# Performance work log

Measured on AMD Instinct MI355X. Metric: run time of the kernel, lower is better.

Reference implementation:

```python
import jax, jax.numpy as jnp
import numpy as np

B, C, T = 32, 32, 1024
K = 64          # kernel_size
DIL = 1         # dilation
MLP_DIM = 256
HID = 256       # mlp_hidden_dim; TanhBlock dims: 256 -> 256 -> 128 -> 1
NF = min(MLP_DIM, K // 2 + 1)          # 33 rfft bins kept
FFT_DIM = C * NF * 2                   # 2112
N_WIN = T - DIL * (K - 1)              # 961 windows


def setup_inputs() -> dict:
    key = jax.random.key(0)
    ks = jax.random.split(key, 8)
    s = 0.02
    return {
        "x": jax.random.normal(ks[0], (B, C, T), dtype=jnp.float32),
        "Wp": jax.random.normal(ks[1], (MLP_DIM, FFT_DIM), dtype=jnp.float32) * s,
        "bp": jnp.zeros((MLP_DIM,), dtype=jnp.float32),
        "W1": jax.random.normal(ks[2], (HID, MLP_DIM), dtype=jnp.float32) * s,
        "b1": jnp.zeros((HID,), dtype=jnp.float32),
        "W2": jax.random.normal(ks[3], (HID // 2, HID), dtype=jnp.float32) * s,
        "b2": jnp.zeros((HID // 2,), dtype=jnp.float32),
        "Wout": jax.random.normal(ks[4], (1, HID // 2), dtype=jnp.float32) * s,
        "bout": jnp.zeros((1,), dtype=jnp.float32),
        "agg": jnp.zeros((N_WIN,), dtype=jnp.float32),
    }


def reference(x, Wp, bp, W1, b1, W2, b2, Wout, bout, agg):
    # Gather all dilated windows at once: window t uses indices (t-start)+k*DIL.
    base = jnp.arange(N_WIN)[:, None] + jnp.arange(K)[None, :] * DIL  # [W, K]
    win = x[:, :, base]                          # [B, C, W, K]
    fft = jnp.fft.rfft(win, axis=-1)[..., :NF]   # [B, C, W, NF] complex
    mag = jnp.log1p(jnp.abs(fft))
    ph = jnp.angle(fft) / np.pi
    feat = jnp.stack([mag, ph], axis=-1)         # [B, C, W, NF, 2]
    # torch reshape order is (C, NF, 2) -> move window axis before channel
    feat = feat.transpose(0, 2, 1, 3, 4).reshape(B, N_WIN, FFT_DIM)  # [B, W, FFT_DIM]
    proj = jnp.tanh(feat @ Wp.T + bp) * np.pi    # [B, W, MLP_DIM]
    h = jnp.tanh(proj @ W1.T + b1)               # [B, W, HID]
    h = jnp.tanh(h @ W2.T + b2)                  # [B, W, HID//2]
    out = (h @ Wout.T + bout)[..., 0]            # [B, W]
    wts = jax.nn.softmax(agg)                    # [W]
    return (out * wts[None, :]).sum(axis=1)      # [B]
```

## Files before the change

kernel.cpp:

```cpp
#include <hip/hip_runtime.h>
#include <math.h>

#define B_   32
#define C_   32
#define T_   1024
#define NF_  33
#define F2_  66
#define FD_  2112
#define NW_  961
#define MLP_ 256
#define HID_ 256
#define HH_  128
#define TN_  32
#define NT_  31

#define PI_F     3.14159265358979323846f
#define LN2_F    0.69314718055994530942f
#define L2E2_F   2.88539008177792681472f

typedef unsigned short u16;
typedef unsigned int   u32;
typedef __attribute__((ext_vector_type(8))) short bf16x8;
typedef __attribute__((ext_vector_type(4))) float f32x4;

__device__ __forceinline__ u16 f2bf(float f) {
    u32 u = __float_as_uint(f);
    u = u + 0x7FFFu + ((u >> 16) & 1u);
    return (u16)(u >> 16);
}
__device__ __forceinline__ float bf2f(u16 h) {
    return __uint_as_float((u32)h << 16);
}
__device__ __forceinline__ void gload16(const void* g, void* l) {
    __builtin_amdgcn_global_load_lds(
        (const __attribute__((address_space(1))) void*)g,
        (__attribute__((address_space(3))) void*)l, 16, 0, 0);
}
__device__ __forceinline__ float ftanh(float x) {
    float z = __builtin_amdgcn_exp2f(x * L2E2_F);
    return 1.f - 2.f * __builtin_amdgcn_rcpf(z + 1.f);
}
__device__ __forceinline__ float flog1p(float x) {
    return __builtin_amdgcn_logf(1.f + x) * LN2_F;
}
__device__ __forceinline__ float fatan2pi(float y, float x) {
    const float ay = fabsf(y), ax = fabsf(x);
    const float mn = fminf(ay, ax), mx = fmaxf(ay, ax);
    float t = mn * __builtin_amdgcn_rcpf(mx);
    t = (mx == 0.f) ? 0.f : t;
    const float s = t * t;
    float p = -0.00373098f;
    p = fmaf(p, s,  0.01676008f);
    p = fmaf(p, s, -0.03706162f);
    p = fmaf(p, s,  0.06160679f);
    p = fmaf(p, s, -0.10587735f);
    p = fmaf(p, s,  0.31830265f);
    p *= t;
    p = (ay > ax) ? 0.5f - p : p;
    p = (x < 0.f) ? 1.0f - p : p;
    return copysignf(p, y);
}

__global__ __launch_bounds__(256) void prep_kernel(
        const float* __restrict__ Wp, const float* __restrict__ W1,
        const float* __restrict__ W2, const float* __restrict__ agg,
        u16* __restrict__ WpH, u16* __restrict__ W1H, u16* __restrict__ W2H,
        float* __restrict__ wts) {
    const int blk = blockIdx.x;
    const int tid = threadIdx.x;
    if (blk < 128) {
        const int total = MLP_ * FD_;
        for (int i = blk * 256 + tid; i < total; i += 128 * 256)
            WpH[i] = f2bf(Wp[i]);
    } else if (blk < 160) {
        const int total = HID_ * MLP_;
        for (int i = (blk - 128) * 256 + tid; i < total; i += 32 * 256)
            W1H[i] = f2bf(W1[i]);
    } else if (blk < 176) {
        const int total = HH_ * HID_;
        for (int i = (blk - 160) * 256 + tid; i < total; i += 16 * 256)
            W2H[i] = f2bf(W2[i]);
    } else {
        __shared__ float red[256];
        float mx = -INFINITY;
        for (int i = tid; i < NW_; i += 256) mx = fmaxf(mx, agg[i]);
        red[tid] = mx; __syncthreads();
        for (int s = 128; s > 0; s >>= 1) {
            if (tid < s) red[tid] = fmaxf(red[tid], red[tid + s]);
            __syncthreads();
        }
        mx = red[0]; __syncthreads();
        float sm = 0.f;
        for (int i = tid; i < NW_; i += 256) sm += expf(agg[i] - mx);
        red[tid] = sm; __syncthreads();
        for (int s = 128; s > 0; s >>= 1) {
            if (tid < s) red[tid] += red[tid + s];
            __syncthreads();
        }
        const float inv = 1.f / red[0];
        for (int i = tid; i < NW_; i += 256) wts[i] = expf(agg[i] - mx) * inv;
    }
}

__global__ __launch_bounds__(256) void feat_kernel(const float* __restrict__ x,
                                                   u32* __restrict__ featP) {
    const int n0 = blockIdx.x * TN_;
    const int cg = blockIdx.y;
    const int bb = blockIdx.z;
    const int tid = threadIdx.x;
    const int tf = tid & 31;
    const int c8 = tid >> 5;
    const int c  = cg * 8 + c8;

    __shared__ float2 stab[64];
    __shared__ float xs[8][96];
    __shared__ float basisT[64][68];

    if (tid < 64) {
        float s, cc;
        sincosf(-PI_F * (float)tid / 32.0f, &s, &cc);
        stab[tid] = make_float2(cc, s);
    }
    __syncthreads();
    for (int e = tid; e < 2048; e += 256) {
        const int f = e >> 6, k = e & 63;
        const float2 w = stab[(f * k) & 63];
        basisT[k][2 * f]     = w.x;
        basisT[k][2 * f + 1] = w.y;
    }
    if (tid < 192) {
        const int cs = tid / 24, q = tid % 24;
        const int t0 = n0 + q * 4;
        const float* xb = x + ((size_t)bb * C_ + cg * 8 + cs) * T_;
        float4 v;
        if (t0 + 3 < T_) {
            v = *(const float4*)(xb + t0);
        } else {
            v.x = (t0 + 0 < T_) ? xb[t0 + 0] : 0.f;
            v.y = (t0 + 1 < T_) ? xb[t0 + 1] : 0.f;
            v.z = (t0 + 2 < T_) ? xb[t0 + 2] : 0.f;
            v.w = 0.f;
        }
        *(float4*)&xs[cs][q * 4] = v;
    }
    __syncthreads();

    const size_t rowb = (size_t)bb * NW_;

    {
        float re = 0.f, im = 0.f;
#pragma unroll
        for (int k = 0; k < 64; ++k) {
            const float xv = xs[c8][k];
            const float2 w = *(const float2*)&basisT[k][2 * tf];
            re = fmaf(xv, w.x, re);
            im = fmaf(xv, w.y, im);
        }
        const float2 st = stab[tf];
        const float cx = st.x, sx = -st.y;

        for (int j = 0; j < TN_; ++j) {
            const int gn = n0 + j;
            if (gn >= NW_) break;
            const float r   = __builtin_amdgcn_sqrtf(re * re + im * im);
            const float mag = flog1p(r);
            const float ph  = fatan2pi(im, re);
            featP[(rowb + gn) * (FD_ / 2) + 33 * c + tf] =
                (u32)f2bf(mag) | ((u32)f2bf(ph) << 16);
            const float tre = re - xs[c8][j] + xs[c8][j + 64];
            re = tre * cx - im * sx;
            im = tre * sx + im * cx;
        }
    }

    {
        const int j   = tid & 31;
        const int c8n = tid >> 5;
        const int gn  = n0 + j;
        if (gn < NW_) {
            float s = 0.f;
#pragma unroll
            for (int k = 0; k < 32; ++k)
                s += xs[c8n][j + 2 * k] - xs[c8n][j + 2 * k + 1];
            const float a = flog1p(fabsf(s));
            const float p = (__float_as_uint(s) >> 31) ? 1.0f : 0.0f;
            featP[(rowb + gn) * (FD_ / 2) + 33 * (cg * 8 + c8n) + 32] =
                (u32)f2bf(a) | ((u32)f2bf(p) << 16);
        }
    }
}

__global__ __launch_bounds__(512, 2) void gemm1t_kernel(
        const u16* __restrict__ A, const u16* __restrict__ BH,
        const float* __restrict__ bias, float scale,
        u16* __restrict__ outH, int Mvalid, int Kd) {
    constexpr int STEPB = 8192 + 16384;
    __shared__ char lds[3 * STEPB];

    const int bm = blockIdx.x;
    const int tid = threadIdx.x;
    const int lane = tid & 63, w = tid >> 6;
    const int wr = w >> 2, wc = w & 3;
    const int m0 = bm * 128;

    f32x4 acc[4][4];
#pragma unroll
    for (int i = 0; i < 4; ++i)
#pragma unroll
        for (int j = 0; j < 4; ++j) acc[i][j] = (f32x4){0.f, 0.f, 0.f, 0.f};

    const size_t rs = (size_t)Kd * 2;
    const char* gA = (const char*)A + (size_t)m0 * rs;
    const char* gB = (const char*)BH;

    auto st1 = [&](const char* g, char* l, int idx) {
        const int row = idx >> 2;
        const int kc  = (idx & 3) ^ ((row >> 1) & 3);
        gload16(g + (size_t)row * rs + (size_t)(kc << 4), l + idx * 16);
    };
    auto stage = [&](int buf, int t) {
        const size_t k0b = (size_t)t << 6;
        char* lb = lds + buf * STEPB;
        st1(gA + k0b, lb, tid);
        st1(gB + k0b, lb + 8192, tid);
        st1(gB + k0b, lb + 8192, tid + 512);
    };

    const int ra_ = wr * 64 + (lane & 15);
    const int rb_ = wc * 64 + (lane & 15);
    const int q   = lane >> 4;
    const int abase = ra_ * 64 + ((q ^ ((ra_ >> 1) & 3)) << 4);
    const int bbase = rb_ * 64 + ((q ^ ((rb_ >> 1) & 3)) << 4);

    const int nt = Kd >> 5;

    stage(0, 0);
    stage(1, 1);

    int cur = 0;
    for (int t = 0; t < nt; ++t) {
        if (t + 1 < nt)
            asm volatile("s_waitcnt vmcnt(3)" ::: "memory");
        else
            asm volatile("s_waitcnt vmcnt(0)" ::: "memory");
        __builtin_amdgcn_sched_barrier(0);
        __builtin_amdgcn_s_barrier();
        asm volatile("" ::: "memory");

        int pf = cur + 2; if (pf >= 3) pf -= 3;
        if (t + 2 < nt) stage(pf, t + 2);

        const char* lb = lds + cur * STEPB;
        bf16x8 a4[4], b4[4];
#pragma unroll
        for (int f = 0; f < 4; ++f) {
            a4[f] = *(const bf16x8*)(lb + abase + f * 1024);
            b4[f] = *(const bf16x8*)(lb + 8192 + bbase + f * 1024);
        }
        __builtin_amdgcn_s_setprio(1);
#pragma unroll
        for (int fm = 0; fm < 4; ++fm)
#pragma unroll
            for (int fn = 0; fn < 4; ++fn)
                acc[fm][fn] = __builtin_amdgcn_mfma_f32_16x16x32_bf16(a4[fm], b4[fn], acc[fm][fn], 0, 0, 0);
        __builtin_amdgcn_s_setprio(0);
        ++cur; if (cur >= 3) cur -= 3;
    }

    float bv[4];
#pragma unroll
    for (int fn = 0; fn < 4; ++fn) bv[fn] = bias[wc * 64 + fn * 16 + (lane & 15)];
#pragma unroll
    for (int fm = 0; fm < 4; ++fm) {
        const int rbase = m0 + wr * 64 + fm * 16 + (lane >> 4) * 4;
#pragma unroll
        for (int fn = 0; fn < 4; ++fn) {
            const int col = wc * 64 + fn * 16 + (lane & 15);
#pragma unroll
            for (int r = 0; r < 4; ++r) {
                const int row = rbase + r;
                if (row < Mvalid) {
                    const float v = ftanh(acc[fm][fn][r] + bv[fn]) * scale;
                    outH[(size_t)row * 256 + col] = f2bf(v);
                }
            }
        }
    }
}

__global__ __launch_bounds__(256, 2) void gemm3f_kernel(
        const u16* __restrict__ A, const u16* __restrict__ BH,
        const float* __restrict__ b2, const float* __restrict__ Wout,
        const float* __restrict__ bout, const float* __restrict__ wts,
        float* __restrict__ partial, int Mvalid, int Kd) {
    constexpr int STEPB = 8192 + 8192;
    __shared__ char lds[3 * STEPB];

    const int bm = blockIdx.x;
    const int tid = threadIdx.x;
    const int lane = tid & 63, w = tid >> 6;
    const int wr = w >> 1, wc = w & 1;
    const int m0 = bm * 128;

    f32x4 acc[4][4];
#pragma unroll
    for (int i = 0; i < 4; ++i)
#pragma unroll
        for (int j = 0; j < 4; ++j) acc[i][j] = (f32x4){0.f, 0.f, 0.f, 0.f};

    const size_t rs = (size_t)Kd * 2;
    const char* gA = (const char*)A + (size_t)m0 * rs;
    const char* gB = (const char*)BH;

    auto st1 = [&](const char* g, char* l, int idx) {
        const int row = idx >> 2;
        const int kc  = (idx & 3) ^ ((row >> 1) & 3);
        gload16(g + (size_t)row * rs + (size_t)(kc << 4), l + idx * 16);
    };
    auto stage = [&](int buf, int t) {
        const size_t k0b = (size_t)t << 6;
        char* lb = lds + buf * STEPB;
        st1(gA + k0b, lb, tid);
        st1(gA + k0b, lb, tid + 256);
        st1(gB + k0b, lb + 8192, tid);
        st1(gB + k0b, lb + 8192, tid + 256);
    };

    const int ra_ = wr * 64 + (lane & 15);
    const int rb_ = wc * 64 + (lane & 15);
    const int q   = lane >> 4;
    const int abase = ra_ * 64 + ((q ^ ((ra_ >> 1) & 3)) << 4);
    const int bbase = rb_ * 64 + ((q ^ ((rb_ >> 1) & 3)) << 4);

    const int nt = Kd >> 5;

    stage(0, 0);
    stage(1, 1);

    int cur = 0;
    for (int t = 0; t < nt; ++t) {
        if (t + 1 < nt)
            asm volatile("s_waitcnt vmcnt(4)" ::: "memory");
        else
            asm volatile("s_waitcnt vmcnt(0)" ::: "memory");
        __builtin_amdgcn_sched_barrier(0);
        __builtin_amdgcn_s_barrier();
        asm volatile("" ::: "memory");

        int pf = cur + 2; if (pf >= 3) pf -= 3;
        if (t + 2 < nt) stage(pf, t + 2);

        const char* lb = lds + cur * STEPB;
        bf16x8 a4[4], b4[4];
#pragma unroll
        for (int f = 0; f < 4; ++f) {
            a4[f] = *(const bf16x8*)(lb + abase + f * 1024);
            b4[f] = *(const bf16x8*)(lb + 8192 + bbase + f * 1024);
        }
        __builtin_amdgcn_s_setprio(1);
#pragma unroll
        for (int fm = 0; fm < 4; ++fm)
#pragma unroll
            for (int fn = 0; fn < 4; ++fn)
                acc[fm][fn] = __builtin_amdgcn_mfma_f32_16x16x32_bf16(a4[fm], b4[fn], acc[fm][fn], 0, 0, 0);
        __builtin_amdgcn_s_setprio(0);
        ++cur; if (cur >= 3) cur -= 3;
    }

    __syncthreads();
    float* rsum = (float*)lds;
    float* red  = (float*)(lds + 1024);

    float bv[4], wv[4];
#pragma unroll
    for (int fn = 0; fn < 4; ++fn) {
        const int col = wc * 64 + fn * 16 + (lane & 15);
        bv[fn] = b2[col];
        wv[fn] = Wout[col];
    }
#pragma unroll
    for (int fm = 0; fm < 4; ++fm) {
#pragma unroll
        for (int r = 0; r < 4; ++r) {
            float c = 0.f;
#pragma unroll
            for (int fn = 0; fn < 4; ++fn)
                c += ftanh(acc[fm][fn][r] + bv[fn]) * wv[fn];
            c += __shfl_xor(c, 1);
            c += __shfl_xor(c, 2);
            c += __shfl_xor(c, 4);
            c += __shfl_xor(c, 8);
            if ((lane & 15) == 0)
                rsum[(wr * 64 + fm * 16 + (lane >> 4) * 4 + r) * 2 + wc] = c;
        }
    }
    __syncthreads();

    const float bO = bout[0];
    float val = 0.f;
    int rowb = -1;
    if (tid < 128) {
        const int gr = m0 + tid;
        if (gr < Mvalid) {
            const float dot = rsum[tid * 2] + rsum[tid * 2 + 1] + bO;
            rowb = gr / NW_;
            val = dot * wts[gr - rowb * NW_];
        }
    }
    __syncthreads();

    const int bFirst = m0 / NW_;
    red[tid] = (tid < 128 && rowb == bFirst) ? val : 0.f;
    __syncthreads();
    for (int s = 128; s > 0; s >>= 1) {
        if (tid < s) red[tid] += red[tid + s];
        __syncthreads();
    }
    if (tid == 0) partial[bm * 2] = red[0];
    __syncthreads();
    red[tid] = (tid < 128 && rowb == bFirst + 1) ? val : 0.f;
    __syncthreads();
    for (int s = 128; s > 0; s >>= 1) {
        if (tid < s) red[tid] += red[tid + s];
        __syncthreads();
    }
    if (tid == 0) partial[bm * 2 + 1] = red[0];
}

__global__ __launch_bounds__(64) void finred_kernel(const float* __restrict__ partial,
                                                    float* __restrict__ out,
                                                    int nbat, int nblocks) {
    const int b = threadIdx.x;
    if (b >= nbat) return;
    int lo = (b * NW_) / 128;
    int hi = ((b + 1) * NW_ - 1) / 128;
    if (hi > nblocks - 1) hi = nblocks - 1;
    float s = 0.f;
    for (int bm = lo; bm <= hi; ++bm) {
        const int slot = ((bm * 128) / NW_ == b) ? 0 : 1;
        s += partial[bm * 2 + slot];
    }
    out[b] = s;
}

extern "C" void kernel_launch(void* const* d_in, const int* in_sizes, int n_in,
                              void* d_out, int out_size, void* d_ws, size_t ws_size,
                              hipStream_t stream) {
    const float* x    = (const float*)d_in[0];
    const float* Wp   = (const float*)d_in[1];
    const float* bp   = (const float*)d_in[2];
    const float* W1   = (const float*)d_in[3];
    const float* b1   = (const float*)d_in[4];
    const float* W2   = (const float*)d_in[5];
    const float* b2   = (const float*)d_in[6];
    const float* Wout = (const float*)d_in[7];
    const float* bout = (const float*)d_in[8];
    const float* agg  = (const float*)d_in[9];
    float* out = (float*)d_out;

    char* wsb = (char*)d_ws;
    size_t off = 0;
    auto ra = [](size_t b) { return (b + 255) & ~(size_t)255; };
    auto alloc = [&](size_t bytes) -> char* {
        char* p = wsb + off;
        off += ra(bytes);
        return p;
    };

    u16* WpH = (u16*)alloc((size_t)MLP_ * FD_ * 2);
    u16* W1H = (u16*)alloc((size_t)HID_ * MLP_ * 2);
    u16* W2H = (u16*)alloc((size_t)HH_ * HID_ * 2);
    float* wts = (float*)alloc((size_t)NW_ * 4);

    const size_t fixed = off;
    int NB = 32;
    for (;;) {
        const size_t M = (size_t)NB * NW_;
        const size_t Mp = ((M + 127) / 128) * 128;
        const size_t need = ra(Mp * FD_ * 2) +
                            ra(Mp * 256 * 2) +
                            ra(Mp * 256 * 2) +
                            ra((Mp / 128) * 2 * 4);
        if (fixed + need <= ws_size || NB == 1) break;
        NB >>= 1;
    }
    const size_t Mmax  = (size_t)NB * NW_;
    const size_t MpMax = ((Mmax + 127) / 128) * 128;
    u16* featH = (u16*)alloc(MpMax * FD_ * 2);
    u16* projH = (u16*)alloc(MpMax * 256 * 2);
    u16* h1H   = (u16*)alloc(MpMax * 256 * 2);
    float* partial = (float*)alloc((MpMax / 128) * 2 * 4);

    prep_kernel<<<dim3(177), dim3(256), 0, stream>>>(
        Wp, W1, W2, agg, WpH, W1H, W2H, wts);

    for (int b0 = 0; b0 < B_; b0 += NB) {
        const int nb = (B_ - b0 < NB) ? (B_ - b0) : NB;
        const int M = nb * NW_;
        const int Mp = ((M + 127) / 128) * 128;

        feat_kernel<<<dim3(NT_, 4, nb), dim3(256), 0, stream>>>(
            x + (size_t)b0 * C_ * T_, (u32*)featH);

        gemm1t_kernel<<<dim3(Mp / 128), dim3(512), 0, stream>>>(
            featH, WpH, bp, PI_F, projH, M, FD_);

        gemm1t_kernel<<<dim3(Mp / 128), dim3(512), 0, stream>>>(
            projH, W1H, b1, 1.0f, h1H, M, MLP_);

        gemm3f_kernel<<<dim3(Mp / 128), dim3(256), 0, stream>>>(
            h1H, W2H, b2, Wout, bout, wts, partial, M, HID_);

        finred_kernel<<<dim3(1), dim3(64), 0, stream>>>(
            partial, out + b0, nb, Mp / 128);
    }
}
```

Measured before the change: 138.3 us.

## Split GEMM N dimension across blocks and pack bf16 with hardware convert

The first two GEMM kernels now use 128x128 output tiles: 256-thread blocks and a second grid dimension over N, instead of 512-thread blocks each covering all 256 output columns. This doubles the number of blocks and shrinks LDS per block, with the launch bounds raised to 3 blocks per CU to improve occupancy and load balance. The cost is that each A tile is loaded twice, once per N half. The feature kernel also switches to the hardware v_cvt_pk_bf16_f32 packed conversion and uses a pointer increment instead of recomputing the index each iteration.

```diff
diff --git a/kernel.cpp b/kernel.cpp
--- a/kernel.cpp
+++ b/kernel.cpp
@@ -30,6 +30,11 @@
 }
 __device__ __forceinline__ float bf2f(u16 h) {
     return __uint_as_float((u32)h << 16);
+}
+__device__ __forceinline__ u32 pk_bf16(float lo, float hi) {
+    u32 r;
+    asm("v_cvt_pk_bf16_f32 %0, %1, %2" : "=v"(r) : "v"(lo), "v"(hi));
+    return r;
 }
 __device__ __forceinline__ void gload16(const void* g, void* l) {
     __builtin_amdgcn_global_load_lds(
@@ -159,14 +164,14 @@
         const float2 st = stab[tf];
         const float cx = st.x, sx = -st.y;
 
-        for (int j = 0; j < TN_; ++j) {
-            const int gn = n0 + j;
-            if (gn >= NW_) break;
-            const float r   = __builtin_amdgcn_sqrtf(re * re + im * im);
+        u32* fp = featP + (rowb + n0) * (FD_ / 2) + 33 * c + tf;
+        const int nw = (NW_ - n0 < TN_) ? (NW_ - n0) : TN_;
+        for (int j = 0; j < nw; ++j) {
+            const float r   = __builtin_amdgcn_sqrtf(fmaf(re, re, im * im));
             const float mag = flog1p(r);
             const float ph  = fatan2pi(im, re);
-            featP[(rowb + gn) * (FD_ / 2) + 33 * c + tf] =
-                (u32)f2bf(mag) | ((u32)f2bf(ph) << 16);
+            *fp = pk_bf16(mag, ph);
+            fp += FD_ / 2;
             const float tre = re - xs[c8][j] + xs[c8][j + 64];
             re = tre * cx - im * sx;
             im = tre * sx + im * cx;
@@ -185,23 +190,23 @@
             const float a = flog1p(fabsf(s));
             const float p = (__float_as_uint(s) >> 31) ? 1.0f : 0.0f;
             featP[(rowb + gn) * (FD_ / 2) + 33 * (cg * 8 + c8n) + 32] =
-                (u32)f2bf(a) | ((u32)f2bf(p) << 16);
-        }
-    }
-}
-
-__global__ __launch_bounds__(512, 2) void gemm1t_kernel(
+                pk_bf16(a, p);
+        }
+    }
+}
+
+__global__ __launch_bounds__(256, 3) void gemm1t_kernel(
         const u16* __restrict__ A, const u16* __restrict__ BH,
         const float* __restrict__ bias, float scale,
-        u16* __restrict__ outH, int Mvalid, int Kd) {
-    constexpr int STEPB = 8192 + 16384;
+        u16* __restrict__ outH, int Mvalid, int Nout, int Kd) {
+    constexpr int STEPB = 8192 + 8192;
     __shared__ char lds[3 * STEPB];
 
-    const int bm = blockIdx.x;
+    const int bm = blockIdx.x, bn = blockIdx.y;
     const int tid = threadIdx.x;
     const int lane = tid & 63, w = tid >> 6;
-    const int wr = w >> 2, wc = w & 3;
-    const int m0 = bm * 128;
+    const int wr = w >> 1, wc = w & 1;
+    const int m0 = bm * 128, n0 = bn * 128;
 
     f32x4 acc[4][4];
 #pragma unroll
@@ -211,7 +216,7 @@
 
     const size_t rs = (size_t)Kd * 2;
     const char* gA = (const char*)A + (size_t)m0 * rs;
-    const char* gB = (const char*)BH;
+    const char* gB = (const char*)BH + (size_t)n0 * rs;
 
     auto st1 = [&](const char* g, char* l, int idx) {
         const int row = idx >> 2;
@@ -222,8 +227,9 @@
         const size_t k0b = (size_t)t << 6;
         char* lb = lds + buf * STEPB;
         st1(gA + k0b, lb, tid);
+        st1(gA + k0b, lb, tid + 256);
         st1(gB + k0b, lb + 8192, tid);
-        st1(gB + k0b, lb + 8192, tid + 512);
+        st1(gB + k0b, lb + 8192, tid + 256);
     };
 
     const int ra_ = wr * 64 + (lane & 15);
@@ -240,7 +246,7 @@
     int cur = 0;
     for (int t = 0; t < nt; ++t) {
         if (t + 1 < nt)
-            asm volatile("s_waitcnt vmcnt(3)" ::: "memory");
+            asm volatile("s_waitcnt vmcnt(4)" ::: "memory");
         else
             asm volatile("s_waitcnt vmcnt(0)" ::: "memory");
         __builtin_amdgcn_sched_barrier(0);
@@ -269,26 +275,26 @@
 
     float bv[4];
 #pragma unroll
-    for (int fn = 0; fn < 4; ++fn) bv[fn] = bias[wc * 64 + fn * 16 + (lane & 15)];
+    for (int fn = 0; fn < 4; ++fn) bv[fn] = bias[n0 + wc * 64 + fn * 16 + (lane & 15)];
 #pragma unroll
     for (int fm = 0; fm < 4; ++fm) {
         const int rbase = m0 + wr * 64 + fm * 16 + (lane >> 4) * 4;
 #pragma unroll
         for (int fn = 0; fn < 4; ++fn) {
-            const int col = wc * 64 + fn * 16 + (lane & 15);
+            const int col = n0 + wc * 64 + fn * 16 + (lane & 15);
 #pragma unroll
             for (int r = 0; r < 4; ++r) {
                 const int row = rbase + r;
                 if (row < Mvalid) {
                     const float v = ftanh(acc[fm][fn][r] + bv[fn]) * scale;
-                    outH[(size_t)row * 256 + col] = f2bf(v);
+                    outH[(size_t)row * Nout + col] = f2bf(v);
                 }
             }
         }
     }
 }
 
-__global__ __launch_bounds__(256, 2) void gemm3f_kernel(
+__global__ __launch_bounds__(256, 3) void gemm3f_kernel(
         const u16* __restrict__ A, const u16* __restrict__ BH,
         const float* __restrict__ b2, const float* __restrict__ Wout,
         const float* __restrict__ bout, const float* __restrict__ wts,
@@ -502,11 +508,11 @@
         feat_kernel<<<dim3(NT_, 4, nb), dim3(256), 0, stream>>>(
             x + (size_t)b0 * C_ * T_, (u32*)featH);
 
-        gemm1t_kernel<<<dim3(Mp / 128), dim3(512), 0, stream>>>(
-            featH, WpH, bp, PI_F, projH, M, FD_);
-
-        gemm1t_kernel<<<dim3(Mp / 128), dim3(512), 0, stream>>>(
-            projH, W1H, b1, 1.0f, h1H, M, MLP_);
+        gemm1t_kernel<<<dim3(Mp / 128, 2), dim3(256), 0, stream>>>(
+            featH, WpH, bp, PI_F, projH, M, MLP_, FD_);
+
+        gemm1t_kernel<<<dim3(Mp / 128, 2), dim3(256), 0, stream>>>(
+            projH, W1H, b1, 1.0f, h1H, M, HID_, MLP_);
 
         gemm3f_kernel<<<dim3(Mp / 128), dim3(256), 0, stream>>>(
             h1H, W2H, b2, Wout, bout, wts, partial, M, HID_);
```

After: 144.7 us. 4.6% more time.

## Fuse second and third MLP GEMMs into one kernel with LDS-resident hidden

Applied to the files above, without the earlier changes.

Merges the W1 GEMM and the W2+Wout reduction into a single kernel. The tanh hidden activations stay in a swizzled 64KB LDS tile instead of round-tripping through global memory, and one kernel launch is removed. It also switches the feature packing to a packed bf16 convert instruction with a pointer-increment store loop. The trade-offs are larger LDS usage, which caps the kernel at one block per CU, and only half the waves doing MFMA work in the second GEMM phase.

```diff
diff --git a/kernel.cpp b/kernel.cpp
--- a/kernel.cpp
+++ b/kernel.cpp
@@ -30,6 +30,11 @@
 }
 __device__ __forceinline__ float bf2f(u16 h) {
     return __uint_as_float((u32)h << 16);
+}
+__device__ __forceinline__ u32 pk_bf16(float lo, float hi) {
+    u32 r;
+    asm("v_cvt_pk_bf16_f32 %0, %1, %2" : "=v"(r) : "v"(lo), "v"(hi));
+    return r;
 }
 __device__ __forceinline__ void gload16(const void* g, void* l) {
     __builtin_amdgcn_global_load_lds(
@@ -159,14 +164,14 @@
         const float2 st = stab[tf];
         const float cx = st.x, sx = -st.y;
 
-        for (int j = 0; j < TN_; ++j) {
-            const int gn = n0 + j;
-            if (gn >= NW_) break;
-            const float r   = __builtin_amdgcn_sqrtf(re * re + im * im);
+        u32* fp = featP + (rowb + n0) * (FD_ / 2) + 33 * c + tf;
+        const int nw = (NW_ - n0 < TN_) ? (NW_ - n0) : TN_;
+        for (int j = 0; j < nw; ++j) {
+            const float r   = __builtin_amdgcn_sqrtf(fmaf(re, re, im * im));
             const float mag = flog1p(r);
             const float ph  = fatan2pi(im, re);
-            featP[(rowb + gn) * (FD_ / 2) + 33 * c + tf] =
-                (u32)f2bf(mag) | ((u32)f2bf(ph) << 16);
+            *fp = pk_bf16(mag, ph);
+            fp += FD_ / 2;
             const float tre = re - xs[c8][j] + xs[c8][j + 64];
             re = tre * cx - im * sx;
             im = tre * sx + im * cx;
@@ -185,7 +190,7 @@
             const float a = flog1p(fabsf(s));
             const float p = (__float_as_uint(s) >> 31) ? 1.0f : 0.0f;
             featP[(rowb + gn) * (FD_ / 2) + 33 * (cg * 8 + c8n) + 32] =
-                (u32)f2bf(a) | ((u32)f2bf(p) << 16);
+                pk_bf16(a, p);
         }
     }
 }
@@ -288,110 +293,192 @@
     }
 }
 
-__global__ __launch_bounds__(256, 2) void gemm3f_kernel(
-        const u16* __restrict__ A, const u16* __restrict__ BH,
+__global__ __launch_bounds__(512, 1) void mlp_tail_kernel(
+        const u16* __restrict__ A, const u16* __restrict__ W1Hp,
+        const float* __restrict__ b1, const u16* __restrict__ W2Hp,
         const float* __restrict__ b2, const float* __restrict__ Wout,
         const float* __restrict__ bout, const float* __restrict__ wts,
-        float* __restrict__ partial, int Mvalid, int Kd) {
-    constexpr int STEPB = 8192 + 8192;
-    __shared__ char lds[3 * STEPB];
+        float* __restrict__ partial, int Mvalid) {
+    constexpr int STEPB = 8192 + 16384;
+    constexpr int OFFX  = 3 * STEPB;
+    __shared__ char lds[OFFX + 65536];
 
     const int bm = blockIdx.x;
     const int tid = threadIdx.x;
     const int lane = tid & 63, w = tid >> 6;
-    const int wr = w >> 1, wc = w & 1;
     const int m0 = bm * 128;
-
-    f32x4 acc[4][4];
+    const size_t rs = 512;
+
+    {
+        const int wr = w >> 2, wc = w & 3;
+        f32x4 acc[4][4];
+#pragma unroll
+        for (int i = 0; i < 4; ++i)
+#pragma unroll
+            for (int j = 0; j < 4; ++j) acc[i][j] = (f32x4){0.f, 0.f, 0.f, 0.f};
+
+        const char* gA = (const char*)A + (size_t)m0 * rs;
+        const char* gB = (const char*)W1Hp;
+
+        auto st1 = [&](const char* g, char* l, int idx) {
+            const int row = idx >> 2;
+            const int kc  = (idx & 3) ^ ((row >> 1) & 3);
+            gload16(g + (size_t)row * rs + (size_t)(kc << 4), l + idx * 16);
+        };
+        auto stage = [&](int buf, int t) {
+            const size_t k0b = (size_t)t << 6;
+            char* lb = lds + buf * STEPB;
+            st1(gA + k0b, lb, tid);
+            st1(gB + k0b, lb + 8192, tid);
+            st1(gB + k0b, lb + 8192, tid + 512);
+        };
+
+        const int ra_ = wr * 64 + (lane & 15);
+        const int rb_ = wc * 64 + (lane & 15);
+        const int q   = lane >> 4;
+        const int abase = ra_ * 64 + ((q ^ ((ra_ >> 1) & 3)) << 4);
+        const int bbase = rb_ * 64 + ((q ^ ((rb_ >> 1) & 3)) << 4);
+
+        stage(0, 0);
+        stage(1, 1);
+
+        int cur = 0;
+        for (int t = 0; t < 8; ++t) {
+            if (t + 1 < 8)
+                asm volatile("s_waitcnt vmcnt(3)" ::: "memory");
+            else
+                asm volatile("s_waitcnt vmcnt(0)" ::: "memory");
+            __builtin_amdgcn_sched_barrier(0);
+            __builtin_amdgcn_s_barrier();
+            asm volatile("" ::: "memory");
+
+            int pf = cur + 2; if (pf >= 3) pf -= 3;
+            if (t + 2 < 8) stage(pf, t + 2);
+
+            const char* lb = lds + cur * STEPB;
+            bf16x8 a4[4], b4[4];
+#pragma unroll
+            for (int f = 0; f < 4; ++f) {
+                a4[f] = *(const bf16x8*)(lb + abase + f * 1024);
+                b4[f] = *(const bf16x8*)(lb + 8192 + bbase + f * 1024);
+            }
+            __builtin_amdgcn_s_setprio(1);
+#pragma unroll
+            for (int fm = 0; fm < 4; ++fm)
+#pragma unroll
+                for (int fn = 0; fn < 4; ++fn)
+                    acc[fm][fn] = __builtin_amdgcn_mfma_f32_16x16x32_bf16(a4[fm], b4[fn], acc[fm][fn], 0, 0, 0);
+            __builtin_amdgcn_s_setprio(0);
+            ++cur; if (cur >= 3) cur -= 3;
+        }
+
+        float bv[4];
+#pragma unroll
+        for (int fn = 0; fn < 4; ++fn) bv[fn] = b1[wc * 64 + fn * 16 + (lane & 15)];
+#pragma unroll
+        for (int fm = 0; fm < 4; ++fm) {
+#pragma unroll
+            for (int fn = 0; fn < 4; ++fn) {
+                const int col = wc * 64 + fn * 16 + (lane & 15);
+                const int cpart = ((col >> 5) << 6) + ((col & 7) * 2);
+                const int kc = (col >> 3) & 3;
+#pragma unroll
+                for (int r = 0; r < 4; ++r) {
+                    const int row = wr * 64 + fm * 16 + (lane >> 4) * 4 + r;
+                    const float v = ftanh(acc[fm][fn][r] + bv[fn]);
+                    const int byt = row * 512 + cpart + ((kc ^ ((row >> 1) & 3)) << 4);
+                    *(u16*)(lds + OFFX + byt) = f2bf(v);
+                }
+            }
+        }
+    }
+    __syncthreads();
+
+    f32x4 acc2[4][4];
 #pragma unroll
     for (int i = 0; i < 4; ++i)
 #pragma unroll
-        for (int j = 0; j < 4; ++j) acc[i][j] = (f32x4){0.f, 0.f, 0.f, 0.f};
-
-    const size_t rs = (size_t)Kd * 2;
-    const char* gA = (const char*)A + (size_t)m0 * rs;
-    const char* gB = (const char*)BH;
-
-    auto st1 = [&](const char* g, char* l, int idx) {
-        const int row = idx >> 2;
-        const int kc  = (idx & 3) ^ ((row >> 1) & 3);
-        gload16(g + (size_t)row * rs + (size_t)(kc << 4), l + idx * 16);
-    };
-    auto stage = [&](int buf, int t) {
-        const size_t k0b = (size_t)t << 6;
-        char* lb = lds + buf * STEPB;
-        st1(gA + k0b, lb, tid);
-        st1(gA + k0b, lb, tid + 256);
-        st1(gB + k0b, lb + 8192, tid);
-        st1(gB + k0b, lb + 8192, tid + 256);
-    };
-
-    const int ra_ = wr * 64 + (lane & 15);
-    const int rb_ = wc * 64 + (lane & 15);
-    const int q   = lane >> 4;
-    const int abase = ra_ * 64 + ((q ^ ((ra_ >> 1) & 3)) << 4);
-    const int bbase = rb_ * 64 + ((q ^ ((rb_ >> 1) & 3)) << 4);
-
-    const int nt = Kd >> 5;
-
-    stage(0, 0);
-    stage(1, 1);
-
-    int cur = 0;
-    for (int t = 0; t < nt; ++t) {
-        if (t + 1 < nt)
-            asm volatile("s_waitcnt vmcnt(4)" ::: "memory");
-        else
-            asm volatile("s_waitcnt vmcnt(0)" ::: "memory");
-        __builtin_amdgcn_sched_barrier(0);
-        __builtin_amdgcn_s_barrier();
-        asm volatile("" ::: "memory");
-
-        int pf = cur + 2; if (pf >= 3) pf -= 3;
-        if (t + 2 < nt) stage(pf, t + 2);
-
-        const char* lb = lds + cur * STEPB;
-        bf16x8 a4[4], b4[4];
-#pragma unroll
-        for (int f = 0; f < 4; ++f) {
-            a4[f] = *(const bf16x8*)(lb + abase + f * 1024);
-            b4[f] = *(const bf16x8*)(lb + 8192 + bbase + f * 1024);
-        }
-        __builtin_amdgcn_s_setprio(1);
-#pragma unroll
-        for (int fm = 0; fm < 4; ++fm)
-#pragma unroll
-            for (int fn = 0; fn < 4; ++fn)
-                acc[fm][fn] = __builtin_amdgcn_mfma_f32_16x16x32_bf16(a4[fm], b4[fn], acc[fm][fn], 0, 0, 0);
-        __builtin_amdgcn_s_setprio(0);
-        ++cur; if (cur >= 3) cur -= 3;
+        for (int j = 0; j < 4; ++j) acc2[i][j] = (f32x4){0.f, 0.f, 0.f, 0.f};
+
+    const int wr2 = (w >> 1) & 1, wc2 = w & 1;
+    {
+        const char* gB2 = (const char*)W2Hp;
+        auto st2 = [&](int buf, int t) {
+            const size_t k0b = (size_t)t << 6;
+            const int row = tid >> 2;
+            const int kc  = (tid & 3) ^ ((row >> 1) & 3);
+            gload16(gB2 + (size_t)row * rs + k0b + (size_t)(kc << 4),
+                    lds + buf * STEPB + tid * 16);
+        };
+        st2(0, 0);
+        st2(1, 1);
+
+        const int q = lane >> 4;
+        const int rb = wc2 * 64 + (lane & 15);
+        const int bbase = rb * 64 + ((q ^ ((rb >> 1) & 3)) << 4);
+        const int ra = wr2 * 64 + (lane & 15);
+        const int abase = ra * 512 + ((q ^ ((ra >> 1) & 3)) << 4);
+
+        int cur = 0;
+        for (int t = 0; t < 8; ++t) {
+            if (t + 1 < 8)
+                asm volatile("s_waitcnt vmcnt(1)" ::: "memory");
+            else
+                asm volatile("s_waitcnt vmcnt(0)" ::: "memory");
+            __builtin_amdgcn_sched_barrier(0);
+            __builtin_amdgcn_s_barrier();
+            asm volatile("" ::: "memory");
+
+            int pf = cur + 2; if (pf >= 3) pf -= 3;
+            if (t + 2 < 8) st2(pf, t + 2);
+
+            if (w < 4) {
+                const char* lb = lds + cur * STEPB;
+                bf16x8 a4[4], b4[4];
+#pragma unroll
+                for (int f = 0; f < 4; ++f) {
+                    a4[f] = *(const bf16x8*)(lds + OFFX + abase + f * 8192 + t * 64);
+                    b4[f] = *(const bf16x8*)(lb + bbase + f * 1024);
+                }
+                __builtin_amdgcn_s_setprio(1);
+#pragma unroll
+                for (int fm = 0; fm < 4; ++fm)
+#pragma unroll
+                    for (int fn = 0; fn < 4; ++fn)
+                        acc2[fm][fn] = __builtin_amdgcn_mfma_f32_16x16x32_bf16(a4[fm], b4[fn], acc2[fm][fn], 0, 0, 0);
+                __builtin_amdgcn_s_setprio(0);
+            }
+            ++cur; if (cur >= 3) cur -= 3;
+        }
     }
 
     __syncthreads();
     float* rsum = (float*)lds;
     float* red  = (float*)(lds + 1024);
 
-    float bv[4], wv[4];
-#pragma unroll
-    for (int fn = 0; fn < 4; ++fn) {
-        const int col = wc * 64 + fn * 16 + (lane & 15);
-        bv[fn] = b2[col];
-        wv[fn] = Wout[col];
-    }
-#pragma unroll
-    for (int fm = 0; fm < 4; ++fm) {
-#pragma unroll
-        for (int r = 0; r < 4; ++r) {
-            float c = 0.f;
-#pragma unroll
-            for (int fn = 0; fn < 4; ++fn)
-                c += ftanh(acc[fm][fn][r] + bv[fn]) * wv[fn];
-            c += __shfl_xor(c, 1);
-            c += __shfl_xor(c, 2);
-            c += __shfl_xor(c, 4);
-            c += __shfl_xor(c, 8);
-            if ((lane & 15) == 0)
-                rsum[(wr * 64 + fm * 16 + (lane >> 4) * 4 + r) * 2 + wc] = c;
+    if (w < 4) {
+        float bv[4], wv[4];
+#pragma unroll
+        for (int fn = 0; fn < 4; ++fn) {
+            const int col = wc2 * 64 + fn * 16 + (lane & 15);
+            bv[fn] = b2[col];
+            wv[fn] = Wout[col];
+        }
+#pragma unroll
+        for (int fm = 0; fm < 4; ++fm) {
+#pragma unroll
+            for (int r = 0; r < 4; ++r) {
+                float c = 0.f;
+#pragma unroll
+                for (int fn = 0; fn < 4; ++fn)
+                    c += ftanh(acc2[fm][fn][r] + bv[fn]) * wv[fn];
+                c += __shfl_xor(c, 1);
+                c += __shfl_xor(c, 2);
+                c += __shfl_xor(c, 4);
+                c += __shfl_xor(c, 8);
+                if ((lane & 15) == 0)
+                    rsum[(wr2 * 64 + fm * 16 + (lane >> 4) * 4 + r) * 2 + wc2] = c;
+            }
         }
     }
     __syncthreads();
@@ -410,7 +497,7 @@
     __syncthreads();
 
     const int bFirst = m0 / NW_;
-    red[tid] = (tid < 128 && rowb == bFirst) ? val : 0.f;
+    if (tid < 256) red[tid] = (tid < 128 && rowb == bFirst) ? val : 0.f;
     __syncthreads();
     for (int s = 128; s > 0; s >>= 1) {
         if (tid < s) red[tid] += red[tid + s];
@@ -418,7 +505,7 @@
     }
     if (tid == 0) partial[bm * 2] = red[0];
     __syncthreads();
-    red[tid] = (tid < 128 && rowb == bFirst + 1) ? val : 0.f;
+    if (tid < 256) red[tid] = (tid < 128 && rowb == bFirst + 1) ? val : 0.f;
     __syncthreads();
     for (int s = 128; s > 0; s >>= 1) {
         if (tid < s) red[tid] += red[tid + s];
@@ -479,7 +566,6 @@
         const size_t Mp = ((M + 127) / 128) * 128;
         const size_t need = ra(Mp * FD_ * 2) +
                             ra(Mp * 256 * 2) +
-                            ra(Mp * 256 * 2) +
                             ra((Mp / 128) * 2 * 4);
         if (fixed + need <= ws_size || NB == 1) break;
         NB >>= 1;
@@ -488,7 +574,6 @@
     const size_t MpMax = ((Mmax + 127) / 128) * 128;
     u16* featH = (u16*)alloc(MpMax * FD_ * 2);
     u16* projH = (u16*)alloc(MpMax * 256 * 2);
-    u16* h1H   = (u16*)alloc(MpMax * 256 * 2);
     float* partial = (float*)alloc((MpMax / 128) * 2 * 4);
 
     prep_kernel<<<dim3(177), dim3(256), 0, stream>>>(
@@ -505,11 +590,8 @@
         gemm1t_kernel<<<dim3(Mp / 128), dim3(512), 0, stream>>>(
             featH, WpH, bp, PI_F, projH, M, FD_);
 
-        gemm1t_kernel<<<dim3(Mp / 128), dim3(512), 0, stream>>>(
-            projH, W1H, b1, 1.0f, h1H, M, MLP_);
-
-        gemm3f_kernel<<<dim3(Mp / 128), dim3(256), 0, stream>>>(
-            h1H, W2H, b2, Wout, bout, wts, partial, M, HID_);
+        mlp_tail_kernel<<<dim3(Mp / 128), dim3(512), 0, stream>>>(
+            projH, W1H, b1, W2H, b2, Wout, bout, wts, partial, M);
 
         finred_kernel<<<dim3(1), dim3(64), 0, stream>>>(
             partial, out + b0, nb, Mp / 128);
```

After: 124.5 us. -10.0%, faster.
